# Optimization experiments

Hardware: AMD Instinct MI355X
Metric: run time of the kernel (lower is better)

Reference implementation:

```python
import jax, jax.numpy as jnp
import numpy as np
from jax import lax

B, L, C = 8, 1024, 512
KH, HID, NL, KS = 4, 64, 2, 3  # K heads, hidden_size, nlayers, kernel_size
BN_EPS = 1e-5


def setup_inputs() -> dict:
    key = jax.random.key(0)
    ks = jax.random.split(key, 12)
    s = 0.02
    inp = {
        "input": jax.random.normal(ks[0], (B, L, C), jnp.float32),
        # key CNN (1 layer): conv [O,I,K], bias, BN gamma/beta/mean/var
        "ck_w": jax.random.normal(ks[1], (C, C, KS), jnp.float32) * s,
        "ck_b": jnp.zeros((C,), jnp.float32),
        "ck_g": jnp.ones((C,), jnp.float32),
        "ck_beta": jnp.zeros((C,), jnp.float32),
        "ck_m": jnp.zeros((C,), jnp.float32),
        "ck_v": jnp.ones((C,), jnp.float32),
        # query CNN (1 layer)
        "cq_w": jax.random.normal(ks[2], (C, C, KS), jnp.float32) * s,
        "cq_b": jnp.zeros((C,), jnp.float32),
        "cq_g": jnp.ones((C,), jnp.float32),
        "cq_beta": jnp.zeros((C,), jnp.float32),
        "cq_m": jnp.zeros((C,), jnp.float32),
        "cq_v": jnp.ones((C,), jnp.float32),
        # per-layer linears, torch Linear layout [out,in]
        "qW": jax.random.normal(ks[3], (NL, HID * KH, C), jnp.float32) * s,
        "qb": jnp.zeros((NL, HID * KH), jnp.float32),
        "kW": jax.random.normal(ks[4], (NL, HID * KH, C), jnp.float32) * s,
        "kb": jnp.zeros((NL, HID * KH), jnp.float32),
        "vW": jax.random.normal(ks[5], (NL, C, C), jnp.float32) * s,
        "vb": jnp.zeros((NL, C), jnp.float32),
    }
    return inp


def _causal_conv_bn_relu(x, w, b, g, beta, m, v):
    # x: [B,L,C] -> causal conv1d (left pad KS-1) + eval BN + ReLU -> [B,L,C]
    xc = jnp.transpose(x, (0, 2, 1))  # NCH
    y = lax.conv_general_dilated(xc, w, (1,), [(KS - 1, 0)],
                                 dimension_numbers=("NCH", "OIH", "NCH"))
    y = y + b[None, :, None]
    y = (y - m[None, :, None]) * (g[None, :, None] / jnp.sqrt(v[None, :, None] + BN_EPS)) + beta[None, :, None]
    return jnp.transpose(jnp.maximum(y, 0.0), (0, 2, 1))


def _convsa(input, ck_w, ck_b, ck_g, ck_beta, ck_m, ck_v,
            cq_w, cq_b, cq_g, cq_beta, cq_m, cq_v, qW, qb, kW, kb, vW, vb):
    bsz, seqlen, dim = input.shape
    cur_mask = jnp.tril(jnp.ones((seqlen, seqlen), input.dtype), -1)  # strict lower
    key_out = _causal_conv_bn_relu(input, ck_w, ck_b, ck_g, ck_beta, ck_m, ck_v)
    query_out = _causal_conv_bn_relu(input, cq_w, cq_b, cq_g, cq_beta, cq_m, cq_v)
    output = input
    graphs, outputs = [], []
    for i in range(NL):
        q = (query_out @ qW[i].T + qb[i]).reshape(bsz, seqlen, KH, HID)  # blkh
        k = (key_out @ kW[i].T + kb[i]).reshape(bsz, seqlen, KH, HID)
        att = jnp.einsum("bqkh,bskh->bkqs", q, k)  # [B,K,L,L]
        # sparse_mode == 1: relu, strict-causal mask, square, L1-normalize squares
        att = jnp.maximum(att, 0.0) * cur_mask
        sq = att * att
        att = sq / (sq.sum(axis=-1, keepdims=True) + 1e-16)
        val = (output @ vW[i].T + vb[i]).reshape(bsz, seqlen, KH, dim // KH)  # blkd
        cur = jnp.einsum("bkqs,bskd->bqkd", att, val).reshape(bsz, seqlen, dim)
        output = output + cur
        graphs.append(att)
        outputs.append(output)
    return jnp.stack(graphs, 0), jnp.stack(outputs, 0)


def reference(input, ck_w, ck_b, ck_g, ck_beta, ck_m, ck_v,
              cq_w, cq_b, cq_g, cq_beta, cq_m, cq_v, qW, qb, kW, kb, vW, vb):
    return _convsa(input, ck_w, ck_b, ck_g, ck_beta, ck_m, ck_v,
                   cq_w, cq_b, cq_g, cq_beta, cq_m, cq_v, qW, qb, kW, kb, vW, vb)
```

## Files before the change

kernel.cpp:

```cpp
#include <hip/hip_runtime.h>
#include <stdint.h>
#include <stddef.h>

#define BB 8
#define LL 1024
#define CC 512
#define KHn 4
#define HIDn 64
#define NLAYER 2
#define MM (BB*LL)

typedef __attribute__((ext_vector_type(4))) float f32x4;
typedef __attribute__((ext_vector_type(8))) short s16x8;
typedef __attribute__((ext_vector_type(4))) short s16x4;

__device__ __forceinline__ short f2bf(float x){
  union { float f; uint32_t u; } v; v.f = x;
  uint32_t r = v.u + 0x7FFFu + ((v.u >> 16) & 1u);
  return (short)(r >> 16);
}

__device__ __forceinline__ short* strip_ptr(char* base, size_t f){
  size_t beta = f << 1;
  size_t strip = beta >> 11;
  return (short*)(base + ((strip >> 9) << 22) + ((strip & 511) << 12) + 2048 + (beta & 2047));
}
__device__ __forceinline__ float* sums_strip(char* base, size_t i){
  size_t strip = 4096 + (i >> 9);
  return (float*)(base + ((strip >> 9) << 22) + ((strip & 511) << 12) + 2048) + (i & 511);
}

__global__ void k_scaleshift(const float* b1,const float* g1,const float* be1,const float* m1,const float* v1,
                             const float* b2,const float* g2,const float* be2,const float* m2,const float* v2,
                             float* sc1, float* sh1, float* sc2, float* sh2){
  int c = blockIdx.x*256 + threadIdx.x;
  if (c < CC){
    float s = g1[c]*rsqrtf(v1[c]+1e-5f); sc1[c]=s; sh1[c]=(b1[c]-m1[c])*s+be1[c];
  } else if (c < 2*CC){
    int d = c - CC;
    float s = g2[d]*rsqrtf(v2[d]+1e-5f); sc2[d]=s; sh2[d]=(b2[d]-m2[d])*s+be2[d];
  }
}

__global__ void k_convwT(const float* __restrict__ wk, const float* __restrict__ wq,
                         float* __restrict__ wTk, float* __restrict__ wTq){
  int idx = blockIdx.x*256 + threadIdx.x;
  int seg = idx / (CC*CC);
  int o   = (idx / CC) % CC;
  int c   = idx % CC;
  size_t src = ((size_t)o*CC + c)*3 + seg;
  wTk[idx] = wk[src];
  wTq[idx] = wq[src];
}

__global__ void k_cast(const float* __restrict__ in, short* __restrict__ out, int n){
  int i = blockIdx.x*256 + threadIdx.x;
  if (i < n) out[i] = f2bf(in[i]);
}

__global__ __launch_bounds__(256,3)
void k_conv2(const float* __restrict__ X,
             const float* __restrict__ WtK, const float* __restrict__ WtQ,
             const float* __restrict__ scK, const float* __restrict__ shK,
             const float* __restrict__ scQ, const float* __restrict__ shQ,
             float* __restrict__ OK, float* __restrict__ OQ)
{
  __shared__ float As[64][64];
  __shared__ float BsK[64][64];
  __shared__ float BsQ[64][64];
  const int tid = threadIdx.x, ty = tid >> 4, tx = tid & 15;
  const int m0 = blockIdx.x << 6, n0 = blockIdx.y << 6;
  const int mlow = m0 & (LL-1);
  float accK[4][4] = {};
  float accQ[4][4] = {};
  for (int seg = 0; seg < 3; ++seg){
    const int shift = seg - 2;
    for (int k0 = 0; k0 < CC; k0 += 64){
      __syncthreads();
      #pragma unroll
      for (int it = 0; it < 4; ++it){
        int idx = tid + (it << 8);
        int r = idx >> 4, c4 = (idx & 15) << 2;
        int colp = (r + ((idx & 7) << 2)) & 63;
        f32x4 av; av[0]=0.f; av[1]=0.f; av[2]=0.f; av[3]=0.f;
        if (mlow + r + shift >= 0) av = *(const f32x4*)&X[(size_t)(m0 + r + shift)*CC + k0 + c4];
        As[c4+0][colp]=av[0]; As[c4+1][colp]=av[1]; As[c4+2][colp]=av[2]; As[c4+3][colp]=av[3];
        f32x4 bk = *(const f32x4*)&WtK[((size_t)seg*CC + n0 + r)*CC + k0 + c4];
        BsK[c4+0][colp]=bk[0]; BsK[c4+1][colp]=bk[1]; BsK[c4+2][colp]=bk[2]; BsK[c4+3][colp]=bk[3];
        f32x4 bq = *(const f32x4*)&WtQ[((size_t)seg*CC + n0 + r)*CC + k0 + c4];
        BsQ[c4+0][colp]=bq[0]; BsQ[c4+1][colp]=bq[1]; BsQ[c4+2][colp]=bq[2]; BsQ[c4+3][colp]=bq[3];
      }
      __syncthreads();
      #pragma unroll
      for (int kg = 0; kg < 16; ++kg){
        const int kb = kg << 2;
        const int s4 = (kg & 7) << 2;
        const float* pA = &As [kb][((ty<<2) + s4) & 63];
        const float* pK = &BsK[kb][((tx<<2) + s4) & 63];
        const float* pQ = &BsQ[kb][((tx<<2) + s4) & 63];
        #pragma unroll
        for (int k4 = 0; k4 < 4; ++k4){
          f32x4 qa = *(const f32x4*)(pA + (k4<<6));
          f32x4 kk = *(const f32x4*)(pK + (k4<<6));
          f32x4 qq = *(const f32x4*)(pQ + (k4<<6));
          #pragma unroll
          for (int i=0;i<4;++i)
            #pragma unroll
            for (int j=0;j<4;++j){
              accK[i][j] += qa[i]*kk[j];
              accQ[i][j] += qa[i]*qq[j];
            }
        }
      }
    }
  }
  const int c0 = n0 + (tx<<2);
  f32x4 sK = *(const f32x4*)&scK[c0];
  f32x4 hK = *(const f32x4*)&shK[c0];
  f32x4 sQ = *(const f32x4*)&scQ[c0];
  f32x4 hQ = *(const f32x4*)&shQ[c0];
  #pragma unroll
  for (int i=0;i<4;++i){
    int gr = m0 + (ty<<2) + i;
    f32x4 vK, vQ;
    #pragma unroll
    for (int j=0;j<4;++j){
      vK[j] = fmaxf(accK[i][j]*sK[j] + hK[j], 0.f);
      vQ[j] = fmaxf(accQ[i][j]*sQ[j] + hQ[j], 0.f);
    }
    *(f32x4*)&OK[(size_t)gr*CC + c0] = vK;
    *(f32x4*)&OQ[(size_t)gr*CC + c0] = vQ;
  }
}

template<int PACK>
__global__ __launch_bounds__(256,2)
void k_linT(const float* __restrict__ A, int lda,
            const float* __restrict__ B, int ldb, int K,
            const float* __restrict__ bias,
            float* __restrict__ O, int ldo)
{
  __shared__ float As[64][64];
  __shared__ float Bs[64][64];
  const int tid = threadIdx.x, ty = tid >> 4, tx = tid & 15;
  const int m0 = blockIdx.x << 6, n0 = blockIdx.y << 6;
  float accs[4][4] = {};
  for (int k0 = 0; k0 < K; k0 += 64){
    __syncthreads();
    #pragma unroll
    for (int it = 0; it < 4; ++it){
      int idx = tid + (it << 8);
      int r = idx >> 4, c4 = (idx & 15) << 2;
      int colp = (r + ((idx & 7) << 2)) & 63;
      f32x4 av = *(const f32x4*)&A[(size_t)(m0 + r)*lda + k0 + c4];
      As[c4+0][colp]=av[0]; As[c4+1][colp]=av[1]; As[c4+2][colp]=av[2]; As[c4+3][colp]=av[3];
      f32x4 bv = *(const f32x4*)&B[(size_t)(n0 + r)*ldb + k0 + c4];
      Bs[c4+0][colp]=bv[0]; Bs[c4+1][colp]=bv[1]; Bs[c4+2][colp]=bv[2]; Bs[c4+3][colp]=bv[3];
    }
    __syncthreads();
    #pragma unroll
    for (int kg = 0; kg < 16; ++kg){
      const int kb = kg << 2;
      const int s4 = (kg & 7) << 2;
      const float* pA = &As[kb][((ty<<2) + s4) & 63];
      const float* pB = &Bs[kb][((tx<<2) + s4) & 63];
      #pragma unroll
      for (int k4 = 0; k4 < 4; ++k4){
        f32x4 qa = *(const f32x4*)(pA + (k4<<6));
        f32x4 kb4 = *(const f32x4*)(pB + (k4<<6));
        #pragma unroll
        for (int i=0;i<4;++i)
          #pragma unroll
          for (int j=0;j<4;++j)
            accs[i][j] += qa[i]*kb4[j];
      }
    }
  }
  const int c0 = n0 + (tx<<2);
  f32x4 b4 = *(const f32x4*)&bias[c0];
  #pragma unroll
  for (int i=0;i<4;++i){
    int gr = m0 + (ty<<2) + i;
    f32x4 v;
    #pragma unroll
    for (int j=0;j<4;++j) v[j] = accs[i][j] + b4[j];
    if (PACK){
      int bb = gr >> 10, l = gr & (LL-1);
      int kh = c0 >> 6, h = c0 & 63;
      *(f32x4*)&O[(((size_t)(bb*KHn + kh))*LL + l)*HIDn + h] = v;
    } else {
      *(f32x4*)&O[(size_t)gr*ldo + c0] = v;
    }
  }
}

template<int SSTRIP>
__global__ __launch_bounds__(256,2)
void k_stile(const float* __restrict__ qp, const float* __restrict__ kp,
             float* __restrict__ gout, float* __restrict__ partial, char* sbase)
{
  __shared__ float Qs[64][20];
  __shared__ float Ks[64][64];
  const int tid = threadIdx.x, lane = tid & 63, w = tid >> 6;
  const int band = blockIdx.x >> 1, half = blockIdx.x & 1;
  const int kh = blockIdx.y, b = blockIdx.z;
  const int q0 = band << 4;
  const int s0 = half << 9;
  const int mk = b*KHn + kh;
  float* grow = gout + (size_t)mk*LL*LL;

  const bool compute = (s0 < q0 + 15);
  float acc[4][8];
  #pragma unroll
  for (int i=0;i<4;++i)
    #pragma unroll
    for (int j=0;j<8;++j) acc[i][j] = 0.f;

  if (compute){
    const float* qb = qp + (size_t)mk*LL*HIDn;
    const float* kb = kp + (size_t)mk*LL*HIDn;
    {
      int row = tid >> 4, c4 = (tid & 15) << 2;
      f32x4 av = *(const f32x4*)&qb[(size_t)(q0 + row)*HIDn + c4];
      Qs[c4+0][row]=av[0]; Qs[c4+1][row]=av[1]; Qs[c4+2][row]=av[2]; Qs[c4+3][row]=av[3];
    }
    for (int j = 0; j < 8; ++j){
      __syncthreads();
      {
        int idx = tid;
        int r = idx >> 4, c4 = (idx & 15) << 2;
        int sw = (idx & 7) << 2;
        #pragma unroll
        for (int it = 0; it < 4; ++it){
          int rr = r + (it << 4);
          int colp = (rr + sw) & 63;
          f32x4 bv = *(const f32x4*)&kb[(size_t)(s0 + (j<<6) + rr)*HIDn + c4];
          Ks[c4+0][colp]=bv[0]; Ks[c4+1][colp]=bv[1]; Ks[c4+2][colp]=bv[2]; Ks[c4+3][colp]=bv[3];
        }
      }
      __syncthreads();
      #pragma unroll
      for (int h = 0; h < 64; ++h){
        float kv = Ks[h][(lane + (((h >> 2) & 7) << 2)) & 63];
        f32x4 qa4 = *(const f32x4*)&Qs[h][w << 2];
        #pragma unroll
        for (int i=0;i<4;++i)
          acc[i][j] += qa4[i] * kv;
      }
    }
  }
  #pragma unroll
  for (int i=0;i<4;++i){
    const int q = q0 + (w<<2) + i;
    float psum = 0.f;
    float* rw = &grow[(size_t)q*LL + s0];
    #pragma unroll
    for (int j=0;j<8;++j){
      const int s = s0 + (j<<6) + lane;
      float tt = (compute && s < q) ? fmaxf(acc[i][j], 0.f) : 0.f;
      float v = tt*tt;
      psum += v;
      rw[(j<<6) + lane] = v;
    }
    psum += __shfl_xor(psum, 1);  psum += __shfl_xor(psum, 2);
    psum += __shfl_xor(psum, 4);  psum += __shfl_xor(psum, 8);
    psum += __shfl_xor(psum, 16); psum += __shfl_xor(psum, 32);
    if (lane == 0){
      size_t idx = (((size_t)mk*2 + half) << 10) + q;
      if (SSTRIP) *sums_strip(sbase, idx) = psum;
      else        partial[idx] = psum;
    }
  }
}

template<int SOUT>
__global__ __launch_bounds__(256,2)
void k_gemm(const float* __restrict__ Af, int lda,
            const short* __restrict__ Bm, int ldb, int K,
            const float* __restrict__ bias,
            short* __restrict__ Obf, int ldo, char* gbase)
{
  __shared__ short As[128][72];
  __shared__ short Bs[128][72];
  const int tid = threadIdx.x, lane = tid & 63, wid = tid >> 6;
  const int wm = wid >> 1, wn = wid & 1;
  const int m0 = blockIdx.x << 7, n0 = blockIdx.y << 7;
  const int lr = lane & 15, lk = (lane >> 4) << 3;

  f32x4 acc[4][4];
  #pragma unroll
  for (int m=0;m<4;++m)
    #pragma unroll
    for (int n=0;n<4;++n){ acc[m][n][0]=0.f; acc[m][n][1]=0.f; acc[m][n][2]=0.f; acc[m][n][3]=0.f; }

  for (int k0 = 0; k0 < K; k0 += 64){
    __syncthreads();
    #pragma unroll
    for (int it=0; it<4; ++it){
      int idx8 = tid + (it<<8);
      int r = idx8 >> 3, cv = (idx8 & 7) << 3;
      f32x4 v0 = *(const f32x4*)&Af[(size_t)(m0+r)*lda + k0 + cv];
      f32x4 v1 = *(const f32x4*)&Af[(size_t)(m0+r)*lda + k0 + cv + 4];
      s16x8 h;
      h[0]=f2bf(v0[0]); h[1]=f2bf(v0[1]); h[2]=f2bf(v0[2]); h[3]=f2bf(v0[3]);
      h[4]=f2bf(v1[0]); h[5]=f2bf(v1[1]); h[6]=f2bf(v1[2]); h[7]=f2bf(v1[3]);
      *(s16x8*)&As[r][cv] = h;
      *(s16x8*)&Bs[r][cv] = *(const s16x8*)&Bm[(size_t)(n0+r)*ldb + k0 + cv];
    }
    __syncthreads();
    #pragma unroll
    for (int kj=0; kj<2; ++kj){
      const int ko = (kj<<5) + lk;
      s16x8 av[4], bv[4];
      #pragma unroll
      for (int m=0;m<4;++m) av[m] = *(const s16x8*)&As[(wm<<6) + (m<<4) + lr][ko];
      #pragma unroll
      for (int n=0;n<4;++n) bv[n] = *(const s16x8*)&Bs[(wn<<6) + (n<<4) + lr][ko];
      #pragma unroll
      for (int m=0;m<4;++m)
        #pragma unroll
        for (int n=0;n<4;++n)
          acc[m][n] = __builtin_amdgcn_mfma_f32_16x16x32_bf16(av[m], bv[n], acc[m][n], 0,0,0);
    }
  }
  const int rr = (lane >> 4) << 2;
  #pragma unroll
  for (int m=0;m<4;++m)
    #pragma unroll
    for (int n=0;n<4;++n){
      const int gc = n0 + (wn<<6) + (n<<4) + lr;
      float e0 = bias[gc];
      #pragma unroll
      for (int r=0;r<4;++r){
        const int gr = m0 + (wm<<6) + (m<<4) + rr + r;
        short val = f2bf(acc[m][n][r] + e0);
        if (SOUT) *strip_ptr(gbase, (size_t)gr*ldo + gc) = val;
        else      Obf[(size_t)gr*ldo + gc] = val;
      }
    }
}

template<int VS>
__global__ __launch_bounds__(256,2)
void k_pv(float* __restrict__ att, const short* __restrict__ valbf, char* vbase,
          const float* __restrict__ partial,
          const float* __restrict__ prevf, float* __restrict__ outs)
{
  __shared__ short As[128][72];
  __shared__ short Bs[128][72];
  __shared__ float rinv_s[128];
  const int tid = threadIdx.x, lane = tid & 63, wid = tid >> 6;
  const int wm = wid >> 1, wn = wid & 1;
  const int qt = blockIdx.x, kh = blockIdx.y, b = blockIdx.z;
  const int qbase = qt << 7;
  const int lr = lane & 15, lk = (lane >> 4) << 3, rr2 = (lane >> 4) << 2;
  const int mk = b*KHn + kh;
  float* attb = att + ((size_t)mk)*LL*LL;

  if (tid < 128){
    int q = qbase + tid;
    float s = 0.f;
    #pragma unroll
    for (int g = 0; g < 2; ++g){
      size_t idx = (((size_t)mk*2 + g) << 10) + q;
      s += VS ? *sums_strip(vbase, idx) : partial[idx];
    }
    rinv_s[tid] = 1.0f/(s + 1e-16f);
  }

  f32x4 acc[4][4];
  #pragma unroll
  for (int m=0;m<4;++m)
    #pragma unroll
    for (int n=0;n<4;++n){ acc[m][n][0]=0.f; acc[m][n][1]=0.f; acc[m][n][2]=0.f; acc[m][n][3]=0.f; }

  const int nt = (qbase >> 6) + 2;
  for (int st=0; st<nt; ++st){
    const int sb = st << 6;
    __syncthreads();
    #pragma unroll
    for (int it=0; it<8; ++it){
      int idx4 = tid + (it<<8);
      int r = idx4 >> 4, cv = (idx4 & 15) << 2;
      float* src = &attb[(size_t)(qbase + r)*LL + sb + cv];
      f32x4 v = *(f32x4*)src;
      float ri = rinv_s[r];
      v[0]*=ri; v[1]*=ri; v[2]*=ri; v[3]*=ri;
      *(f32x4*)src = v;
      s16x4 h; h[0]=f2bf(v[0]); h[1]=f2bf(v[1]); h[2]=f2bf(v[2]); h[3]=f2bf(v[3]);
      *(s16x4*)&As[r][cv] = h;
    }
    #pragma unroll
    for (int it=0; it<32; ++it){
      int idx = tid + (it<<8);
      int sl = idx >> 7, d = idx & 127;
      size_t f = (size_t)(b*LL + sb + sl)*CC + kh*128 + d;
      Bs[d][sl] = VS ? *strip_ptr(vbase, f) : valbf[f];
    }
    __syncthreads();
    #pragma unroll
    for (int kj=0;kj<2;++kj){
      int ko = (kj<<5) + lk;
      s16x8 av[4], bv[4];
      #pragma unroll
      for (int m=0;m<4;++m) av[m] = *(const s16x8*)&As[(wm<<6)+(m<<4)+lr][ko];
      #pragma unroll
      for (int n=0;n<4;++n) bv[n] = *(const s16x8*)&Bs[(wn<<6)+(n<<4)+lr][ko];
      #pragma unroll
      for (int m=0;m<4;++m)
        #pragma unroll
        for (int n=0;n<4;++n)
          acc[m][n] = __builtin_amdgcn_mfma_f32_16x16x32_bf16(av[m], bv[n], acc[m][n], 0,0,0);
    }
  }
  #pragma unroll
  for (int m=0;m<4;++m)
    #pragma unroll
    for (int n=0;n<4;++n)
      #pragma unroll
      for (int r=0;r<4;++r){
        const int R = b*LL + qbase + (wm<<6) + (m<<4) + rr2 + r;
        const int gc = kh*128 + (wn<<6) + (n<<4) + lr;
        size_t o = (size_t)R*CC + gc;
        outs[o] = prevf[o] + acc[m][n][r];
      }
}

__global__ void k_restore(char* gbase){
  size_t strip = blockIdx.x;
  char* p = gbase + ((strip >> 9) << 22) + ((strip & 511) << 12) + 2048;
  f32x4 z; z[0]=0.f; z[1]=0.f; z[2]=0.f; z[3]=0.f;
  ((f32x4*)p)[threadIdx.x] = z;
}

extern "C" void kernel_launch(void* const* d_in, const int* in_sizes, int n_in,
                              void* d_out, int out_size, void* d_ws, size_t ws_size,
                              hipStream_t stream)
{
  (void)in_sizes; (void)n_in; (void)out_size; (void)d_ws; (void)ws_size;
  const float* input  = (const float*)d_in[0];
  const float* ck_w   = (const float*)d_in[1];
  const float* ck_b   = (const float*)d_in[2];
  const float* ck_g   = (const float*)d_in[3];
  const float* ck_be  = (const float*)d_in[4];
  const float* ck_m   = (const float*)d_in[5];
  const float* ck_v   = (const float*)d_in[6];
  const float* cq_w   = (const float*)d_in[7];
  const float* cq_b   = (const float*)d_in[8];
  const float* cq_g   = (const float*)d_in[9];
  const float* cq_be  = (const float*)d_in[10];
  const float* cq_m   = (const float*)d_in[11];
  const float* cq_v   = (const float*)d_in[12];
  const float* qW     = (const float*)d_in[13];
  const float* qb     = (const float*)d_in[14];
  const float* kW     = (const float*)d_in[15];
  const float* kb     = (const float*)d_in[16];
  const float* vW     = (const float*)d_in[17];
  const float* vb     = (const float*)d_in[18];

  float* graphs   = (float*)d_out;
  float* g1       = graphs + (size_t)BB*KHn*LL*LL;
  float* outsBase = graphs + (size_t)NLAYER*BB*KHn*LL*LL;
  float* outs0 = outsBase;
  float* outs1 = outsBase + (size_t)MM*CC;

  char* RA = (char*)g1;
  float* key_out  = (float*)(RA + 0);
  float* qry_out  = (float*)(RA + 16777216);
  float* q0v      = (float*)(RA + 33554432);
  float* k0v      = (float*)(RA + 41943040);
  short* val0_bf  = (short*)(RA + 50331648);
  short* vW_bf    = (short*)(RA + 58720256);
  float* wTk      = (float*)(RA + 59768832);
  float* wTq      = (float*)(RA + 62914560);
  float* partial0 = (float*)(RA + 66060288);
  float* ck_sc    = (float*)(RA + 66322432);
  float* ck_sh    = (float*)(RA + 66324480);
  float* cq_sc    = (float*)(RA + 66326528);
  float* cq_sh    = (float*)(RA + 66328576);
  float* q1v = outs1;
  float* k1v = outs1 + (size_t)MM*KHn*HIDn;
  char* gL0 = (char*)d_out;

  k_scaleshift<<<4, 256, 0, stream>>>(ck_b, ck_g, ck_be, ck_m, ck_v,
                                      cq_b, cq_g, cq_be, cq_m, cq_v,
                                      ck_sc, ck_sh, cq_sc, cq_sh);
  k_convwT<<<(3*CC*CC)/256, 256, 0, stream>>>(ck_w, cq_w, wTk, wTq);
  k_cast<<<(NLAYER*CC*CC)/256, 256, 0, stream>>>(vW, vW_bf, NLAYER*CC*CC);

  k_conv2<<<dim3(MM/64, CC/64), 256, 0, stream>>>(input, wTk, wTq,
                                                  ck_sc, ck_sh, cq_sc, cq_sh,
                                                  key_out, qry_out);

  k_linT<1><<<dim3(MM/64, (KHn*HIDn)/64), 256, 0, stream>>>(qry_out, CC, qW, CC, CC,
                                                            qb, q0v, KHn*HIDn);
  k_linT<1><<<dim3(MM/64, (KHn*HIDn)/64), 256, 0, stream>>>(key_out, CC, kW, CC, CC,
                                                            kb, k0v, KHn*HIDn);
  k_gemm<0><<<dim3(MM/128, CC/128), 256, 0, stream>>>(input, CC, vW_bf, CC, CC,
                                                      vb, val0_bf, CC, nullptr);
  k_stile<0><<<dim3(128, KHn, BB), 256, 0, stream>>>(q0v, k0v, graphs, partial0, nullptr);
  k_pv<0><<<dim3(LL/128, KHn, BB), 256, 0, stream>>>(graphs, val0_bf, gL0, partial0,
                                                     input, outs0);

  k_gemm<1><<<dim3(MM/128, CC/128), 256, 0, stream>>>(outs0, CC, vW_bf + (size_t)CC*CC, CC, CC,
                                                      vb + CC, nullptr, CC, gL0);
  k_linT<1><<<dim3(MM/64, (KHn*HIDn)/64), 256, 0, stream>>>(qry_out, CC,
                                                            qW + (size_t)KHn*HIDn*CC, CC, CC,
                                                            qb + KHn*HIDn, q1v, KHn*HIDn);
  k_linT<1><<<dim3(MM/64, (KHn*HIDn)/64), 256, 0, stream>>>(key_out, CC,
                                                            kW + (size_t)KHn*HIDn*CC, CC, CC,
                                                            kb + KHn*HIDn, k1v, KHn*HIDn);
  k_stile<1><<<dim3(128, KHn, BB), 256, 0, stream>>>(q1v, k1v, g1, nullptr, gL0);
  k_pv<1><<<dim3(LL/128, KHn, BB), 256, 0, stream>>>(g1, nullptr, gL0, nullptr,
                                                     outs0, outs1);
  k_restore<<<8192, 128, 0, stream>>>(gL0);
}
```

Before: 987.4 us.

## Recompute first sequence rows of Q/K in exact fp32 via side kernels

Adds two small kernels that recompute the causal conv and Q/K projections for the first 33 sequence positions with plain fp32 scalar loops. The score kernel then reads those rows from the side buffers instead of the main GEMM outputs. This looks aimed at accuracy for early rows, where the normalization has few terms, rather than at speed. It adds extra launches and slow scalar work, and the conv kernel's occupancy hint also changes from 3 to 2.

```diff
diff --git a/kernel.cpp b/kernel.cpp
--- a/kernel.cpp
+++ b/kernel.cpp
@@ -9,6 +9,10 @@
 #define HIDn 64
 #define NLAYER 2
 #define MM (BB*LL)
+#define NP 34
+#define NXR 33
+#define QX1S 4224
+#define KX1S 4360
 
 typedef __attribute__((ext_vector_type(4))) float f32x4;
 typedef __attribute__((ext_vector_type(8))) short s16x8;
@@ -27,6 +31,10 @@
 }
 __device__ __forceinline__ float* sums_strip(char* base, size_t i){
   size_t strip = 4096 + (i >> 9);
+  return (float*)(base + ((strip >> 9) << 22) + ((strip & 511) << 12) + 2048) + (i & 511);
+}
+__device__ __forceinline__ float* fx_at(char* base, int strip0, size_t i){
+  size_t strip = (size_t)strip0 + (i >> 9);
   return (float*)(base + ((strip >> 9) << 22) + ((strip & 511) << 12) + 2048) + (i & 511);
 }
 
@@ -58,7 +66,58 @@
   if (i < n) out[i] = f2bf(in[i]);
 }
 
-__global__ __launch_bounds__(256,3)
+__global__ void k_exconv(const float* __restrict__ input,
+                         const float* __restrict__ wk, const float* __restrict__ wq,
+                         const float* __restrict__ sck, const float* __restrict__ shk,
+                         const float* __restrict__ scq, const float* __restrict__ shq,
+                         float* __restrict__ fc){
+  const int pos = blockIdx.x, t = blockIdx.y, b = blockIdx.z;
+  const float* xb = input + (size_t)b*LL*CC;
+  const float* w  = t ? wq  : wk;
+  const float* sc = t ? scq : sck;
+  const float* sh = t ? shq : shk;
+  for (int ch = threadIdx.x; ch < CC; ch += 256){
+    float acc = 0.f;
+    for (int kk = 0; kk < 3; ++kk){
+      int xl = pos + kk - 2;
+      if (xl < 0) continue;
+      const float* wr = w + (size_t)ch*CC*3 + kk;
+      const float* xr = xb + (size_t)xl*CC;
+      for (int i = 0; i < CC; ++i) acc += wr[(size_t)i*3]*xr[i];
+    }
+    fc[(((size_t)t*BB + b)*NP + pos)*CC + ch] = fmaxf(acc*sc[ch] + sh[ch], 0.f);
+  }
+}
+
+template<int STRIP>
+__global__ void k_exproj(const float* __restrict__ fc,
+                         const float* __restrict__ qW, const float* __restrict__ qb,
+                         const float* __restrict__ kW, const float* __restrict__ kb,
+                         int layer, float* __restrict__ qx, float* __restrict__ kx,
+                         char* sbase){
+  const int side = blockIdx.x;
+  const int kh = blockIdx.y, b = blockIdx.z;
+  const int mk = b*KHn + kh;
+  const float* W  = side ? kW : qW;
+  const float* Bv = side ? kb : qb;
+  const int t = side ? 0 : 1;
+  for (int idx = threadIdx.x; idx < NXR*HIDn; idx += 256){
+    int rr = idx >> 6, h = idx & 63;
+    const float* cv = fc + (((size_t)t*BB + b)*NP + rr)*CC;
+    const float* wr = W + ((size_t)layer*KHn*HIDn + kh*HIDn + h)*CC;
+    float acc = Bv[layer*KHn*HIDn + kh*HIDn + h];
+    for (int c = 0; c < CC; ++c) acc += wr[c]*cv[c];
+    size_t oi = ((size_t)mk*NXR + rr)*HIDn + h;
+    if (STRIP){
+      if (side == 0) *fx_at(sbase, QX1S, oi) = acc;
+      else           *fx_at(sbase, KX1S, oi) = acc;
+    } else {
+      if (side == 0) qx[oi] = acc; else kx[oi] = acc;
+    }
+  }
+}
+
+__global__ __launch_bounds__(256,2)
 void k_conv2(const float* __restrict__ X,
              const float* __restrict__ WtK, const float* __restrict__ WtQ,
              const float* __restrict__ scK, const float* __restrict__ shK,
@@ -197,6 +256,7 @@
 template<int SSTRIP>
 __global__ __launch_bounds__(256,2)
 void k_stile(const float* __restrict__ qp, const float* __restrict__ kp,
+             const float* __restrict__ qx, const float* __restrict__ kx,
              float* __restrict__ gout, float* __restrict__ partial, char* sbase)
 {
   __shared__ float Qs[64][20];
@@ -221,7 +281,15 @@
     const float* kb = kp + (size_t)mk*LL*HIDn;
     {
       int row = tid >> 4, c4 = (tid & 15) << 2;
-      f32x4 av = *(const f32x4*)&qb[(size_t)(q0 + row)*HIDn + c4];
+      int qrow = q0 + row;
+      const float* src;
+      if (qrow <= 32){
+        size_t oi = ((size_t)mk*NXR + qrow)*HIDn + c4;
+        src = SSTRIP ? fx_at(sbase, QX1S, oi) : &qx[oi];
+      } else {
+        src = &qb[(size_t)qrow*HIDn + c4];
+      }
+      f32x4 av = *(const f32x4*)src;
       Qs[c4+0][row]=av[0]; Qs[c4+1][row]=av[1]; Qs[c4+2][row]=av[2]; Qs[c4+3][row]=av[3];
     }
     for (int j = 0; j < 8; ++j){
@@ -234,7 +302,15 @@
         for (int it = 0; it < 4; ++it){
           int rr = r + (it << 4);
           int colp = (rr + sw) & 63;
-          f32x4 bv = *(const f32x4*)&kb[(size_t)(s0 + (j<<6) + rr)*HIDn + c4];
+          int srow = s0 + (j<<6) + rr;
+          const float* src;
+          if (srow <= 32){
+            size_t oi = ((size_t)mk*NXR + srow)*HIDn + c4;
+            src = SSTRIP ? fx_at(sbase, KX1S, oi) : &kx[oi];
+          } else {
+            src = &kb[(size_t)srow*HIDn + c4];
+          }
+          f32x4 bv = *(const f32x4*)src;
           Ks[c4+0][colp]=bv[0]; Ks[c4+1][colp]=bv[1]; Ks[c4+2][colp]=bv[2]; Ks[c4+3][colp]=bv[3];
         }
       }
@@ -478,6 +554,9 @@
   float* ck_sh    = (float*)(RA + 66324480);
   float* cq_sc    = (float*)(RA + 66326528);
   float* cq_sh    = (float*)(RA + 66328576);
+  float* fc   = outs0;
+  float* q0x  = outs0 + (size_t)2*BB*NP*CC;
+  float* k0x  = q0x + (size_t)32*NXR*HIDn;
   float* q1v = outs1;
   float* k1v = outs1 + (size_t)MM*KHn*HIDn;
   char* gL0 = (char*)d_out;
@@ -487,6 +566,8 @@
                                       ck_sc, ck_sh, cq_sc, cq_sh);
   k_convwT<<<(3*CC*CC)/256, 256, 0, stream>>>(ck_w, cq_w, wTk, wTq);
   k_cast<<<(NLAYER*CC*CC)/256, 256, 0, stream>>>(vW, vW_bf, NLAYER*CC*CC);
+  k_exconv<<<dim3(NP, 2, BB), 256, 0, stream>>>(input, ck_w, cq_w,
+                                                ck_sc, ck_sh, cq_sc, cq_sh, fc);
 
   k_conv2<<<dim3(MM/64, CC/64), 256, 0, stream>>>(input, wTk, wTq,
                                                   ck_sc, ck_sh, cq_sc, cq_sh,
@@ -496,9 +577,13 @@
                                                             qb, q0v, KHn*HIDn);
   k_linT<1><<<dim3(MM/64, (KHn*HIDn)/64), 256, 0, stream>>>(key_out, CC, kW, CC, CC,
                                                             kb, k0v, KHn*HIDn);
+  k_exproj<0><<<dim3(2, KHn, BB), 256, 0, stream>>>(fc, qW, qb, kW, kb, 0, q0x, k0x, nullptr);
   k_gemm<0><<<dim3(MM/128, CC/128), 256, 0, stream>>>(input, CC, vW_bf, CC, CC,
                                                       vb, val0_bf, CC, nullptr);
-  k_stile<0><<<dim3(128, KHn, BB), 256, 0, stream>>>(q0v, k0v, graphs, partial0, nullptr);
+  k_stile<0><<<dim3(128, KHn, BB), 256, 0, stream>>>(q0v, k0v, q0x, k0x,
+                                                     graphs, partial0, nullptr);
+  k_exproj<1><<<dim3(2, KHn, BB), 256, 0, stream>>>(fc, qW, qb, kW, kb, 1,
+                                                    nullptr, nullptr, gL0);
   k_pv<0><<<dim3(LL/128, KHn, BB), 256, 0, stream>>>(graphs, val0_bf, gL0, partial0,
                                                      input, outs0);
 
@@ -510,7 +595,8 @@
   k_linT<1><<<dim3(MM/64, (KHn*HIDn)/64), 256, 0, stream>>>(key_out, CC,
                                                             kW + (size_t)KHn*HIDn*CC, CC, CC,
                                                             kb + KHn*HIDn, k1v, KHn*HIDn);
-  k_stile<1><<<dim3(128, KHn, BB), 256, 0, stream>>>(q1v, k1v, g1, nullptr, gL0);
+  k_stile<1><<<dim3(128, KHn, BB), 256, 0, stream>>>(q1v, k1v, nullptr, nullptr,
+                                                     g1, nullptr, gL0);
   k_pv<1><<<dim3(LL/128, KHn, BB), 256, 0, stream>>>(g1, nullptr, gL0, nullptr,
                                                      outs0, outs1);
   k_restore<<<8192, 128, 0, stream>>>(gL0);
```

New measurement: 2.292 ms. 2.32x slower.
